# Performance work log

Measured on AMD Instinct MI355X. Metric: run time of the kernel, lower is better.

Reference implementation:

```python
import jax, jax.numpy as jnp
import numpy as np

EPS = 1e-8
BETA = 1.0
NUM_ITEM = 100000
DIM = 256
NUM_SETS = 8192
SET_LEN = 50
BATCH = 131072


def _init_table(key, clamp_min=None):
    w = 0.1 * jax.random.normal(key, (NUM_ITEM, DIM), dtype=jnp.float32)
    nrm = jnp.linalg.norm(w, axis=1, keepdims=True)
    w = w / jnp.maximum(nrm, 1.0)
    if clamp_min is not None:
        w = jnp.maximum(w, clamp_min)
    return w


def setup_inputs() -> dict:
    key = jax.random.key(0)
    ks = jax.random.split(key, 8)
    S = jax.random.randint(ks[0], (NUM_SETS, SET_LEN), 0, NUM_ITEM, dtype=jnp.int64 if jax.config.jax_enable_x64 else jnp.int32)
    M = jax.random.randint(ks[1], (NUM_SETS, SET_LEN), 0, 2, dtype=jnp.int32)
    instances = jax.random.randint(ks[2], (BATCH, 2), 0, NUM_SETS, dtype=jnp.int32)
    similarities = jax.random.uniform(ks[3], (BATCH, 4), dtype=jnp.float32)
    stdv = 1.0 / np.sqrt(DIM)
    center_att = jax.random.uniform(ks[4], (DIM,), minval=-stdv, maxval=stdv, dtype=jnp.float32)
    radius_att = jax.random.uniform(ks[5], (DIM,), minval=-stdv, maxval=stdv, dtype=jnp.float32)
    center_w = _init_table(ks[6])
    radius_w = _init_table(ks[7], clamp_min=EPS)
    return {"S": S, "M": M, "instances": instances, "similarities": similarities,
            "center_w": center_w, "radius_w": radius_w,
            "center_att": center_att, "radius_att": radius_att}


def _softplus_beta(x):
    # f.softplus(x, beta) = log(1 + exp(beta*x)) / beta
    return jax.nn.softplus(BETA * x) / BETA


def _attention_ber(S, M, X, A):
    # Dense masked equivalent of nonzero() + scatter_softmax + scatter_sum.
    att = X @ A                              # [num_item]
    logits = att[S]                          # [num_sets, L]
    mask = M > 0
    logits = jnp.where(mask, logits, -1e30)
    w = jax.nn.softmax(logits, axis=1)       # [num_sets, L]
    w = jnp.where(mask, w, 0.0)
    emb = jnp.einsum('sl,sld->sd', w, X[S])  # [num_sets, D]
    sizes = jnp.sum(M, axis=1).astype(X.dtype)  # set sizes
    emb = emb * (sizes[:, None] ** (1.0 / DIM))  # size_reg=True for both
    return emb


def reference(S, M, instances, similarities, center_w, radius_w, center_att, radius_att):
    emb_c_all = _attention_ber(S, M, center_w, center_att)   # [num_sets, D]
    emb_r_all = _attention_ber(S, M, radius_w, radius_att)   # [num_sets, D]
    emb_center = emb_c_all[instances]  # [B, 2, D]
    emb_radius = emb_r_all[instances]  # [B, 2, D]

    c_i, c_j = emb_center[:, 0, :], emb_center[:, 1, :]
    r_i, r_j = emb_radius[:, 0, :], emb_radius[:, 1, :]
    m_i, m_j = c_i, c_j
    M_i, M_j = c_i + r_i, c_j + r_j

    box_volume_i = jnp.sum(jnp.log(_softplus_beta(r_i) + EPS), axis=1)
    box_volume_j = jnp.sum(jnp.log(_softplus_beta(r_j) + EPS), axis=1)
    box_volume_mul_ij = box_volume_i + box_volume_j
    box_inter = jnp.sum(jnp.log(_softplus_beta(jnp.minimum(M_i, M_j) - jnp.maximum(m_i, m_j)) + EPS), axis=1)
    box_union = jnp.sum(jnp.log(_softplus_beta(jnp.maximum(M_i, M_j) - jnp.minimum(m_i, m_j)) + EPS), axis=1)

    c_overlap = jnp.exp(box_inter - jnp.maximum(box_volume_i, box_volume_j))
    c_jaccard = jnp.exp(box_inter - box_union)
    c_cosine = jnp.exp(box_inter - box_volume_mul_ij / 2)
    c_dice = 2 * jnp.exp(box_inter) / (jnp.exp(box_volume_i) + jnp.exp(box_volume_j) + EPS)

    lose_1 = jnp.sum((c_overlap - similarities[:, 0]) ** 2)
    lose_2 = jnp.sum((c_jaccard - similarities[:, 1]) ** 2)
    lose_3 = jnp.sum((c_cosine - similarities[:, 2]) ** 2)
    lose_4 = jnp.sum((c_dice - similarities[:, 3]) ** 2)
    return (lose_1, lose_2, lose_3, lose_4)
```

## Files before the change

### kernel.cpp

```cpp
#include <hip/hip_runtime.h>

#define EPSF 1e-8f
#define DIM 256
#define SET_LEN 50
#define NUM_SETS 8192
#define BATCH 131072

#define LOG2E 1.4426950408889634f
#define LN2   0.6931471805599453f
#define EPS2  1.4426950409e-8f
#define CPD  -0.5287663729448977f

#define QSCALE 100.0f
#define QINV   0.01f
#define Q2E    (QINV * LOG2E)
#define LUTOFF 204
#define LUTSZ  512

#define SSCALE 127.0f
#define SINV   (1.0f / 127.0f)

#define PPW 16
#define NPAIRBLK (BATCH / (PPW * 4))

__device__ __forceinline__ float fast_exp2(float x) {
#if __has_builtin(__builtin_amdgcn_exp2f)
    return __builtin_amdgcn_exp2f(x);
#else
    return exp2f(x);
#endif
}
__device__ __forceinline__ float fast_log2(float x) {
#if __has_builtin(__builtin_amdgcn_logf)
    return __builtin_amdgcn_logf(x);
#else
    return __log2f(x);
#endif
}

__device__ __forceinline__ float lsp2(float x) {
    float e = fast_exp2(x * LOG2E);
    float s = fast_log2(1.0f + e);
    return fast_log2(s + EPS2);
}
__device__ __forceinline__ float lsp2q(int q) {
    float e = fast_exp2((float)q * Q2E);
    float s = fast_log2(1.0f + e);
    return fast_log2(s + EPS2);
}

__device__ __forceinline__ float wave_reduce_sum(float v) {
    #pragma unroll
    for (int off = 32; off > 0; off >>= 1) v += __shfl_xor(v, off, 64);
    return v;
}
__device__ __forceinline__ float wave_reduce_max(float v) {
    #pragma unroll
    for (int off = 32; off > 0; off >>= 1) v = fmaxf(v, __shfl_xor(v, off, 64));
    return v;
}

__device__ __forceinline__ float dot4(float4 a, float4 b) {
    return a.x*b.x + a.y*b.y + a.z*b.z + a.w*b.w;
}
__device__ __forceinline__ signed char quant8(float v) {
    int q = (int)rintf(v * QSCALE);
    q = max(-127, min(127, q));
    return (signed char)q;
}
__device__ __forceinline__ unsigned int pack_i8x4(float4 v) {
    int a = max(-127, min(127, (int)rintf(v.x * SSCALE)));
    int b = max(-127, min(127, (int)rintf(v.y * SSCALE)));
    int c = max(-127, min(127, (int)rintf(v.z * SSCALE)));
    int d = max(-127, min(127, (int)rintf(v.w * SSCALE)));
    return (unsigned int)(a & 0xff) | ((unsigned int)(b & 0xff) << 8) |
           ((unsigned int)(c & 0xff) << 16) | ((unsigned int)(d & 0xff) << 24);
}

__global__ __launch_bounds__(256) void attn_kernel(
    const int* __restrict__ S, const int* __restrict__ M,
    const float* __restrict__ Xc, const float* __restrict__ Xr,
    const float* __restrict__ Ac, const float* __restrict__ Ar,
    signed char* __restrict__ emb_q, float* __restrict__ bv)
{
    const int s    = blockIdx.x;
    const int tid  = threadIdx.x;
    const int lane = tid & 63;
    const int wid  = tid >> 6;
    const int g    = lane >> 4;
    const int sl   = lane & 15;

    __shared__ signed char shc[SET_LEN][DIM];
    __shared__ signed char shr[SET_LEN][DIM];
    __shared__ int   sh_act[SET_LEN];
    __shared__ float sh_wc[SET_LEN];
    __shared__ float sh_wr[SET_LEN];
    __shared__ int   sh_nact;
    __shared__ float sh_scale;
    __shared__ float sh_red[4];

    if (wid == 0) {
        int idx = 0, m = 0;
        if (lane < SET_LEN) {
            idx = S[s * SET_LEN + lane];
            m   = M[s * SET_LEN + lane];
        }
        unsigned long long bal = __ballot(m != 0);
        int rank = __popcll(bal & ((1ull << lane) - 1ull));
        if (m) sh_act[rank] = idx;
        if (lane == 0) {
            int n = __popcll(bal);
            sh_nact = n;
            sh_scale = (n > 0) ? exp2f(log2f((float)n) * (1.0f / DIM)) : 0.0f;
        }
    }
    __syncthreads();
    const int nact = sh_nact;

    float4 afc[4], afr[4];
    #pragma unroll
    for (int c = 0; c < 4; ++c) {
        afc[c] = ((const float4*)Ac)[c * 16 + sl];
        afr[c] = ((const float4*)Ar)[c * 16 + sl];
    }

    const int nit = (nact + 15) >> 4;
    for (int it = 0; it < nit; ++it) {
        const int k = it * 16 + wid * 4 + g;
        float pc = 0.0f, pr = 0.0f;
        if (k < nact) {
            const size_t row = (size_t)sh_act[k] * DIM;
            const float4* xc = (const float4*)(Xc + row);
            const float4* xr = (const float4*)(Xr + row);
            float4 c0 = xc[sl], c1 = xc[16 + sl], c2 = xc[32 + sl], c3 = xc[48 + sl];
            float4 r0 = xr[sl], r1 = xr[16 + sl], r2 = xr[32 + sl], r3 = xr[48 + sl];
            pc = dot4(c0, afc[0]) + dot4(c1, afc[1]) + dot4(c2, afc[2]) + dot4(c3, afc[3]);
            pr = dot4(r0, afr[0]) + dot4(r1, afr[1]) + dot4(r2, afr[2]) + dot4(r3, afr[3]);
            *(unsigned int*)&shc[k][  0 + 4*sl] = pack_i8x4(c0);
            *(unsigned int*)&shc[k][ 64 + 4*sl] = pack_i8x4(c1);
            *(unsigned int*)&shc[k][128 + 4*sl] = pack_i8x4(c2);
            *(unsigned int*)&shc[k][192 + 4*sl] = pack_i8x4(c3);
            *(unsigned int*)&shr[k][  0 + 4*sl] = pack_i8x4(r0);
            *(unsigned int*)&shr[k][ 64 + 4*sl] = pack_i8x4(r1);
            *(unsigned int*)&shr[k][128 + 4*sl] = pack_i8x4(r2);
            *(unsigned int*)&shr[k][192 + 4*sl] = pack_i8x4(r3);
        }
        #pragma unroll
        for (int off = 8; off > 0; off >>= 1) {
            pc += __shfl_xor(pc, off, 64);
            pr += __shfl_xor(pr, off, 64);
        }
        if (k < nact && sl == 0) { sh_wc[k] = pc; sh_wr[k] = pr; }
    }
    __syncthreads();

    if (wid < 2) {
        float* w = (wid == 0) ? sh_wc : sh_wr;
        float v  = (lane < nact) ? w[lane] : -1e30f;
        float mx = wave_reduce_max(v);
        float p  = (lane < nact) ? __expf(v - mx) : 0.0f;
        float sm = wave_reduce_sum(p);
        float inv = (sm > 0.0f) ? (1.0f / sm) : 0.0f;
        if (lane < nact) w[lane] = p * inv;
    }
    __syncthreads();

    float accc = 0.0f, accr = 0.0f;
    #pragma unroll 4
    for (int k = 0; k < nact; ++k) {
        accc = fmaf(sh_wc[k], (float)shc[k][tid], accc);
        accr = fmaf(sh_wr[k], (float)shr[k][tid], accr);
    }
    const float scale = sh_scale * SINV;
    const float ec = accc * scale;
    const float er = accr * scale;
    emb_q[(size_t)s * 512 + tid]       = quant8(ec);
    emb_q[(size_t)s * 512 + 256 + tid] = quant8(er);

    float term = lsp2(er);
    float wsum = wave_reduce_sum(term);
    if (lane == 0) sh_red[wid] = wsum;
    __syncthreads();
    if (tid == 0)
        bv[s] = LN2 * ((sh_red[0] + sh_red[1] + sh_red[2] + sh_red[3])
                       + (float)DIM * CPD);
}

__device__ __forceinline__ void i8x16_unpack(uint4 u, int* o) {
    unsigned int ws[4] = { u.x, u.y, u.z, u.w };
    #pragma unroll
    for (int w = 0; w < 4; ++w) {
        o[4*w+0] = (int)(signed char)(ws[w]);
        o[4*w+1] = (int)(signed char)(ws[w] >> 8);
        o[4*w+2] = (int)(signed char)(ws[w] >> 16);
        o[4*w+3] = (int)(signed char)(ws[w] >> 24);
    }
}

__device__ __forceinline__ void pair_accum_lut(const float* __restrict__ lut,
                                               uint4 ac, uint4 ar, uint4 bc, uint4 br,
                                               float& it, float& ut) {
    int ci[16], ri[16], cj[16], rj[16];
    i8x16_unpack(ac, ci); i8x16_unpack(ar, ri);
    i8x16_unpack(bc, cj); i8x16_unpack(br, rj);
    #pragma unroll
    for (int k = 0; k < 16; ++k) {
        const int Mi = ci[k] + ri[k];
        const int Mj = cj[k] + rj[k];
        const int lo = min(Mi, Mj) - max(ci[k], cj[k]);
        const int hi = max(Mi, Mj) - min(ci[k], cj[k]);
        it += lut[lo + LUTOFF];
        ut += lut[hi + LUTOFF];
    }
}

__global__ __launch_bounds__(256) void pair_kernel(
    const int* __restrict__ inst, const float* __restrict__ sims,
    const signed char* __restrict__ emb_q,
    const float* __restrict__ bv, float4* __restrict__ part)
{
    const int tid  = threadIdx.x;
    const int lane = tid & 63;
    const int wid  = tid >> 6;
    const int g    = lane >> 4;
    const int sl   = lane & 15;
    const int wave = blockIdx.x * 4 + wid;
    const int base = wave * PPW;

    __shared__ float lut[LUTSZ];
    __shared__ float sh_i[4][PPW];
    __shared__ float sh_u[4][PPW];
    __shared__ float sred[4][4];

    #pragma unroll
    for (int e = tid; e < LUTSZ; e += 256) lut[e] = lsp2q(e - LUTOFF);

    int idxreg = 0;
    if (lane < 2 * PPW) idxreg = inst[2 * base + lane];
    __syncthreads();

    uint4 a_c, a_r, b_c, b_r;
    {
        const int i = __shfl(idxreg, 2 * g);
        const int j = __shfl(idxreg, 2 * g + 1);
        const uint4* pi = (const uint4*)(emb_q + (size_t)i * 512);
        const uint4* pj = (const uint4*)(emb_q + (size_t)j * 512);
        a_c = pi[sl]; a_r = pi[16 + sl];
        b_c = pj[sl]; b_r = pj[16 + sl];
    }

    #pragma unroll
    for (int m = 0; m < 4; ++m) {
        uint4 n0, n1, n2, n3;
        if (m < 3) {
            const int slot = (m + 1) * 4 + g;
            const int i = __shfl(idxreg, 2 * slot);
            const int j = __shfl(idxreg, 2 * slot + 1);
            const uint4* pi = (const uint4*)(emb_q + (size_t)i * 512);
            const uint4* pj = (const uint4*)(emb_q + (size_t)j * 512);
            n0 = pi[sl]; n1 = pi[16 + sl];
            n2 = pj[sl]; n3 = pj[16 + sl];
        }

        float it = 0.0f, ut = 0.0f;
        pair_accum_lut(lut, a_c, a_r, b_c, b_r, it, ut);
        #pragma unroll
        for (int o = 8; o > 0; o >>= 1) {
            it += __shfl_xor(it, o, 64);
            ut += __shfl_xor(ut, o, 64);
        }
        if (sl == 0) { sh_i[wid][m * 4 + g] = it; sh_u[wid][m * 4 + g] = ut; }

        if (m < 3) { a_c = n0; a_r = n1; b_c = n2; b_r = n3; }
    }
    __syncthreads();

    float l1 = 0.0f, l2 = 0.0f, l3 = 0.0f, l4 = 0.0f;
    if (lane < PPW) {
        const int b = base + lane;
        const int i = inst[2 * b];
        const int j = inst[2 * b + 1];
        const float inter = LN2 * (sh_i[wid][lane] + (float)DIM * CPD);
        const float unn   = LN2 * (sh_u[wid][lane] + (float)DIM * CPD);
        const float bvi = bv[i], bvj = bv[j];
        const float co  = __expf(inter - fmaxf(bvi, bvj));
        const float cja = __expf(inter - unn);
        const float cco = __expf(inter - 0.5f * (bvi + bvj));
        const float cdi = 2.0f * __expf(inter) /
                          (__expf(bvi) + __expf(bvj) + EPSF);
        const float4 sm = ((const float4*)sims)[b];
        float d;
        d = co  - sm.x; l1 = d * d;
        d = cja - sm.y; l2 = d * d;
        d = cco - sm.z; l3 = d * d;
        d = cdi - sm.w; l4 = d * d;
    }
    l1 = wave_reduce_sum(l1);
    l2 = wave_reduce_sum(l2);
    l3 = wave_reduce_sum(l3);
    l4 = wave_reduce_sum(l4);

    if (lane == 0) {
        sred[wid][0] = l1; sred[wid][1] = l2;
        sred[wid][2] = l3; sred[wid][3] = l4;
    }
    __syncthreads();
    if (tid == 0) {
        float4 p;
        p.x = sred[0][0] + sred[1][0] + sred[2][0] + sred[3][0];
        p.y = sred[0][1] + sred[1][1] + sred[2][1] + sred[3][1];
        p.z = sred[0][2] + sred[1][2] + sred[2][2] + sred[3][2];
        p.w = sred[0][3] + sred[1][3] + sred[2][3] + sred[3][3];
        part[blockIdx.x] = p;
    }
}

__global__ __launch_bounds__(256) void reduce_out(
    const float4* __restrict__ part, float* __restrict__ out)
{
    const int tid  = threadIdx.x;
    const int lane = tid & 63;
    const int wid  = tid >> 6;

    double s0 = 0.0, s1 = 0.0, s2 = 0.0, s3 = 0.0;
    for (int k = tid; k < NPAIRBLK; k += 256) {
        float4 p = part[k];
        s0 += (double)p.x; s1 += (double)p.y;
        s2 += (double)p.z; s3 += (double)p.w;
    }
    #pragma unroll
    for (int off = 32; off > 0; off >>= 1) {
        s0 += __shfl_xor(s0, off, 64);
        s1 += __shfl_xor(s1, off, 64);
        s2 += __shfl_xor(s2, off, 64);
        s3 += __shfl_xor(s3, off, 64);
    }
    __shared__ double sd[4][4];
    if (lane == 0) { sd[wid][0] = s0; sd[wid][1] = s1; sd[wid][2] = s2; sd[wid][3] = s3; }
    __syncthreads();
    if (tid == 0) {
        out[0] = (float)(sd[0][0] + sd[1][0] + sd[2][0] + sd[3][0]);
        out[1] = (float)(sd[0][1] + sd[1][1] + sd[2][1] + sd[3][1]);
        out[2] = (float)(sd[0][2] + sd[1][2] + sd[2][2] + sd[3][2]);
        out[3] = (float)(sd[0][3] + sd[1][3] + sd[2][3] + sd[3][3]);
    }
}

extern "C" void kernel_launch(void* const* d_in, const int* in_sizes, int n_in,
                              void* d_out, int out_size, void* d_ws, size_t ws_size,
                              hipStream_t stream) {
    const int*   S    = (const int*)d_in[0];
    const int*   M    = (const int*)d_in[1];
    const int*   inst = (const int*)d_in[2];
    const float* sims = (const float*)d_in[3];
    const float* Xc   = (const float*)d_in[4];
    const float* Xr   = (const float*)d_in[5];
    const float* Ac   = (const float*)d_in[6];
    const float* Ar   = (const float*)d_in[7];
    float* out = (float*)d_out;

    char* ws = (char*)d_ws;
    signed char* emb_q = (signed char*)(ws);
    float*  bv   = (float*)(ws + 4194304);
    float4* part = (float4*)(ws + 4227072);

    attn_kernel<<<NUM_SETS, 256, 0, stream>>>(S, M, Xc, Xr, Ac, Ar, emb_q, bv);
    pair_kernel<<<NPAIRBLK, 256, 0, stream>>>(inst, sims, emb_q, bv, part);
    reduce_out<<<1, 256, 0, stream>>>(part, out);
}
```

Measured before the change: 87.41 us.

## Split attention kernel into separate center and radius blocks per set

The attention kernel now launches two blocks per set, one for the center table and one for the radius table, instead of one block handling both. Each block keeps half the shared memory and per-thread state, which should raise occupancy and parallelism for the gather-bound stage. The cost is that every set's index and mask loading, ballot compaction and softmax setup now run twice. The box-volume reduction is done only in the radius block.

```diff
diff --git a/kernel.cpp b/kernel.cpp
--- a/kernel.cpp
+++ b/kernel.cpp
@@ -83,18 +83,21 @@
     const float* __restrict__ Ac, const float* __restrict__ Ar,
     signed char* __restrict__ emb_q, float* __restrict__ bv)
 {
-    const int s    = blockIdx.x;
+    const int blk  = blockIdx.x;
+    const int s    = blk >> 1;
+    const int t    = blk & 1;
     const int tid  = threadIdx.x;
     const int lane = tid & 63;
     const int wid  = tid >> 6;
     const int g    = lane >> 4;
     const int sl   = lane & 15;
 
-    __shared__ signed char shc[SET_LEN][DIM];
-    __shared__ signed char shr[SET_LEN][DIM];
+    const float* __restrict__ X = t ? Xr : Xc;
+    const float* __restrict__ A = t ? Ar : Ac;
+
+    __shared__ signed char sh[SET_LEN][DIM];
     __shared__ int   sh_act[SET_LEN];
-    __shared__ float sh_wc[SET_LEN];
-    __shared__ float sh_wr[SET_LEN];
+    __shared__ float sh_w[SET_LEN];
     __shared__ int   sh_nact;
     __shared__ float sh_scale;
     __shared__ float sh_red[4];
@@ -117,73 +120,57 @@
     __syncthreads();
     const int nact = sh_nact;
 
-    float4 afc[4], afr[4];
-    #pragma unroll
-    for (int c = 0; c < 4; ++c) {
-        afc[c] = ((const float4*)Ac)[c * 16 + sl];
-        afr[c] = ((const float4*)Ar)[c * 16 + sl];
-    }
+    float4 af[4];
+    #pragma unroll
+    for (int c = 0; c < 4; ++c) af[c] = ((const float4*)A)[c * 16 + sl];
 
     const int nit = (nact + 15) >> 4;
     for (int it = 0; it < nit; ++it) {
         const int k = it * 16 + wid * 4 + g;
-        float pc = 0.0f, pr = 0.0f;
+        float p = 0.0f;
         if (k < nact) {
             const size_t row = (size_t)sh_act[k] * DIM;
-            const float4* xc = (const float4*)(Xc + row);
-            const float4* xr = (const float4*)(Xr + row);
-            float4 c0 = xc[sl], c1 = xc[16 + sl], c2 = xc[32 + sl], c3 = xc[48 + sl];
-            float4 r0 = xr[sl], r1 = xr[16 + sl], r2 = xr[32 + sl], r3 = xr[48 + sl];
-            pc = dot4(c0, afc[0]) + dot4(c1, afc[1]) + dot4(c2, afc[2]) + dot4(c3, afc[3]);
-            pr = dot4(r0, afr[0]) + dot4(r1, afr[1]) + dot4(r2, afr[2]) + dot4(r3, afr[3]);
-            *(unsigned int*)&shc[k][  0 + 4*sl] = pack_i8x4(c0);
-            *(unsigned int*)&shc[k][ 64 + 4*sl] = pack_i8x4(c1);
-            *(unsigned int*)&shc[k][128 + 4*sl] = pack_i8x4(c2);
-            *(unsigned int*)&shc[k][192 + 4*sl] = pack_i8x4(c3);
-            *(unsigned int*)&shr[k][  0 + 4*sl] = pack_i8x4(r0);
-            *(unsigned int*)&shr[k][ 64 + 4*sl] = pack_i8x4(r1);
-            *(unsigned int*)&shr[k][128 + 4*sl] = pack_i8x4(r2);
-            *(unsigned int*)&shr[k][192 + 4*sl] = pack_i8x4(r3);
+            const float4* x = (const float4*)(X + row);
+            float4 v0 = x[sl], v1 = x[16 + sl], v2 = x[32 + sl], v3 = x[48 + sl];
+            p = dot4(v0, af[0]) + dot4(v1, af[1]) + dot4(v2, af[2]) + dot4(v3, af[3]);
+            *(unsigned int*)&sh[k][  0 + 4*sl] = pack_i8x4(v0);
+            *(unsigned int*)&sh[k][ 64 + 4*sl] = pack_i8x4(v1);
+            *(unsigned int*)&sh[k][128 + 4*sl] = pack_i8x4(v2);
+            *(unsigned int*)&sh[k][192 + 4*sl] = pack_i8x4(v3);
         }
         #pragma unroll
-        for (int off = 8; off > 0; off >>= 1) {
-            pc += __shfl_xor(pc, off, 64);
-            pr += __shfl_xor(pr, off, 64);
-        }
-        if (k < nact && sl == 0) { sh_wc[k] = pc; sh_wr[k] = pr; }
-    }
-    __syncthreads();
-
-    if (wid < 2) {
-        float* w = (wid == 0) ? sh_wc : sh_wr;
-        float v  = (lane < nact) ? w[lane] : -1e30f;
+        for (int off = 8; off > 0; off >>= 1)
+            p += __shfl_xor(p, off, 64);
+        if (k < nact && sl == 0) sh_w[k] = p;
+    }
+    __syncthreads();
+
+    if (wid == 0) {
+        float v  = (lane < nact) ? sh_w[lane] : -1e30f;
         float mx = wave_reduce_max(v);
         float p  = (lane < nact) ? __expf(v - mx) : 0.0f;
         float sm = wave_reduce_sum(p);
         float inv = (sm > 0.0f) ? (1.0f / sm) : 0.0f;
-        if (lane < nact) w[lane] = p * inv;
-    }
-    __syncthreads();
-
-    float accc = 0.0f, accr = 0.0f;
+        if (lane < nact) sh_w[lane] = p * inv;
+    }
+    __syncthreads();
+
+    float acc = 0.0f;
     #pragma unroll 4
-    for (int k = 0; k < nact; ++k) {
-        accc = fmaf(sh_wc[k], (float)shc[k][tid], accc);
-        accr = fmaf(sh_wr[k], (float)shr[k][tid], accr);
-    }
-    const float scale = sh_scale * SINV;
-    const float ec = accc * scale;
-    const float er = accr * scale;
-    emb_q[(size_t)s * 512 + tid]       = quant8(ec);
-    emb_q[(size_t)s * 512 + 256 + tid] = quant8(er);
-
-    float term = lsp2(er);
-    float wsum = wave_reduce_sum(term);
-    if (lane == 0) sh_red[wid] = wsum;
-    __syncthreads();
-    if (tid == 0)
-        bv[s] = LN2 * ((sh_red[0] + sh_red[1] + sh_red[2] + sh_red[3])
-                       + (float)DIM * CPD);
+    for (int k = 0; k < nact; ++k)
+        acc = fmaf(sh_w[k], (float)sh[k][tid], acc);
+    const float e = acc * sh_scale * SINV;
+    emb_q[(size_t)s * 512 + t * 256 + tid] = quant8(e);
+
+    if (t) {
+        float term = lsp2(e);
+        float wsum = wave_reduce_sum(term);
+        if (lane == 0) sh_red[wid] = wsum;
+        __syncthreads();
+        if (tid == 0)
+            bv[s] = LN2 * ((sh_red[0] + sh_red[1] + sh_red[2] + sh_red[3])
+                           + (float)DIM * CPD);
+    }
 }
 
 __device__ __forceinline__ void i8x16_unpack(uint4 u, int* o) {
@@ -364,7 +351,7 @@
     float*  bv   = (float*)(ws + 4194304);
     float4* part = (float4*)(ws + 4227072);
 
-    attn_kernel<<<NUM_SETS, 256, 0, stream>>>(S, M, Xc, Xr, Ac, Ar, emb_q, bv);
+    attn_kernel<<<2 * NUM_SETS, 256, 0, stream>>>(S, M, Xc, Xr, Ac, Ar, emb_q, bv);
     pair_kernel<<<NPAIRBLK, 256, 0, stream>>>(inst, sims, emb_q, bv, part);
     reduce_out<<<1, 256, 0, stream>>>(part, out);
 }
```

Result: no change. 86.94 us (median of 2 runs) (-0.5%).
